# Performance work log

Measured on AMD Instinct MI355X. Metric: run time of the kernel, lower is better.

Reference implementation:

```python
import jax, jax.numpy as jnp
import numpy as np

D = 1024
H = 16
DH = D // H  # 64


def setup_inputs() -> dict:
    key = jax.random.key(0)
    ks = jax.random.split(key, 11)
    B, T = 4, 2048
    s = 1.0 / np.sqrt(D)
    return {
        "q": jax.random.normal(ks[0], (B, T, D), jnp.float32),
        "k": jax.random.normal(ks[1], (B, T, D), jnp.float32),
        "v": jax.random.normal(ks[2], (B, T, D), jnp.float32),
        "Wq": jax.random.normal(ks[3], (D, D), jnp.float32) * s,
        "bq": jnp.zeros((D,), jnp.float32),
        "Wk": jax.random.normal(ks[4], (D, D), jnp.float32) * s,
        "bk": jnp.zeros((D,), jnp.float32),
        "Wv": jax.random.normal(ks[5], (D, D), jnp.float32) * s,
        "bv": jnp.zeros((D,), jnp.float32),
        "gamma": jnp.ones((D,), jnp.float32),
        "beta": jnp.zeros((D,), jnp.float32),
    }


def _layernorm(x, gamma, beta, eps=1e-8):
    # torch LayerNorm variant: unbiased std, eps added to std (not var)
    mean = jnp.mean(x, axis=-1, keepdims=True)
    var = jnp.sum((x - mean) ** 2, axis=-1, keepdims=True) / (x.shape[-1] - 1)
    std = jnp.sqrt(var)
    return gamma * (x - mean) / (std + eps) + beta


def reference(q, k, v, Wq, bq, Wk, bk, Wv, bv, gamma, beta):
    B, T, _ = q.shape
    # projections (D -> D)
    q_ = q @ Wq + bq
    k_ = k @ Wk + bk
    v_ = v @ Wv + bv
    # head split: chunk(dim=2) + cat(dim=0)  ==  (B,T,H,dh) -> (H,B,T,dh)
    qh = q_.reshape(B, T, H, DH).transpose(2, 0, 1, 3)
    kh = k_.reshape(B, T, H, DH).transpose(2, 0, 1, 3)
    vh = v_.reshape(B, T, H, DH).transpose(2, 0, 1, 3)
    scores = jnp.einsum("hbqd,hbkd->hbqk", qh, kh) / jnp.sqrt(
        jnp.asarray(DH, qh.dtype)
    )
    attn = jax.nn.softmax(scores, axis=-1)
    out = jnp.einsum("hbqk,hbkd->hbqd", attn, vh)  # (H,B,T,dh)
    # merge heads: chunk(dim=0) + cat(dim=2)
    out = out.transpose(1, 2, 0, 3).reshape(B, T, D)
    return _layernorm(out + q, gamma, beta)
```

## Files before the change

kernel.cpp:

```cpp
#include <hip/hip_runtime.h>

constexpr int B  = 4;
constexpr int T  = 2048;
constexpr int D  = 1024;
constexpr int H  = 16;
constexpr int DH = 64;
constexpr int BT = B * T;


typedef __attribute__((ext_vector_type(8))) short bf16x8;
typedef __attribute__((ext_vector_type(4))) float f32x4;
typedef __attribute__((ext_vector_type(4))) unsigned short u16x4;
typedef __attribute__((ext_vector_type(4))) unsigned int u32x4;

static __device__ __forceinline__ unsigned short f2bf(float f) {
    unsigned u = __builtin_bit_cast(unsigned, f);
    unsigned r = (u + 0x7fffu + ((u >> 16) & 1u)) >> 16;
    return (unsigned short)r;
}

static __device__ __forceinline__ unsigned cvt_pk_bf16(float lo, float hi) {
    unsigned r;
    asm("v_cvt_pk_bf16_f32 %0, %1, %2" : "=v"(r) : "v"(lo), "v"(hi));
    return r;
}

static __device__ __forceinline__ void pl32swap(unsigned &a, unsigned &b) {
    asm volatile("v_permlane32_swap_b32 %0, %1" : "+v"(a), "+v"(b));
}
static __device__ __forceinline__ void pl16swap(unsigned &a, unsigned &b) {
    asm volatile("v_permlane16_swap_b32 %0, %1" : "+v"(a), "+v"(b));
}

static __device__ __forceinline__ void stage16(const unsigned short* g, unsigned short* l) {
    __builtin_amdgcn_global_load_lds(
        (const __attribute__((address_space(1))) unsigned int*)g,
        (__attribute__((address_space(3))) unsigned int*)l, 16, 0, 0);
}

__global__ __launch_bounds__(256) void transpose_w(
    const float* __restrict__ Wq,
    const float* __restrict__ Wk,
    const float* __restrict__ Wv,
    unsigned short* __restrict__ WT) {
    __shared__ unsigned short tile[32][33];
    const float* src = (blockIdx.y == 0) ? Wq : (blockIdx.y == 1) ? Wk : Wv;
    unsigned short* dst = WT + (size_t)blockIdx.y * D * D;
    int tx = blockIdx.x % (D / 32);
    int ty = blockIdx.x / (D / 32);
    int c  = threadIdx.x & 31;
    int r0 = threadIdx.x >> 5;
#pragma unroll
    for (int i = 0; i < 4; i++) {
        int r = r0 + i * 8;
        tile[r][c] = f2bf(src[(size_t)(ty * 32 + r) * D + tx * 32 + c]);
    }
    __syncthreads();
#pragma unroll
    for (int i = 0; i < 4; i++) {
        int r = r0 + i * 8;
        dst[(size_t)(tx * 32 + r) * D + ty * 32 + c] = tile[c][r];
    }
}

__global__ __launch_bounds__(256, 4) void qkv_gemm_fused(
    const float* __restrict__ Xq,
    const float* __restrict__ Xk,
    const float* __restrict__ Xv,
    const unsigned short* __restrict__ WTall,
    const float* __restrict__ bq,
    const float* __restrict__ bk,
    const float* __restrict__ bv,
    unsigned short* __restrict__ Qp,
    unsigned short* __restrict__ Kp,
    unsigned short* __restrict__ Vt) {
    __shared__ __align__(16) unsigned short Als[128 * 64];
    __shared__ __align__(16) unsigned short Bls[128 * 64];

    const int which = blockIdx.y;
    const float* X = (which == 0) ? Xq : (which == 1) ? Xk : Xv;
    const unsigned short* Wt = WTall + (size_t)which * D * D;
    const float* bias = (which == 0) ? bq : (which == 1) ? bk : bv;

    int bx = blockIdx.x;
    int sb   = (bx & 7) * 64 + (bx >> 3);
    int nblk = sb & 7;
    int mblk = sb >> 3;
    int tid  = threadIdx.x;
    int wave = tid >> 6, lane = tid & 63;
    int lane15 = lane & 15, quad = lane >> 4;
    int wm = (wave >> 1) * 64;
    int wn = (wave & 1) * 64;

    const size_t m0 = (size_t)mblk * 128;
    const size_t n0 = (size_t)nblk * 128;

    f32x4 acc[4][4] = {};

    for (int kt = 0; kt < D / 64; kt++) {
        int k0 = kt * 64;
#pragma unroll
        for (int i = 0; i < 4; i++) {
            int gl  = i * 256 + tid;
            int row = gl >> 3, c = gl & 7;
            int sg  = c ^ (row & 7);
            stage16(Wt + (n0 + row) * D + k0 + sg * 8,
                    Bls + (size_t)(i * 256 + wave * 64) * 8);
        }
        f32x4 xa[4][2];
#pragma unroll
        for (int j = 0; j < 4; j++) {
            int id  = j * 256 + tid;
            int row = id >> 3, c = id & 7;
            int sg  = c ^ (row & 7);
            const float* src = X + (m0 + row) * D + k0 + sg * 8;
            xa[j][0] = *(const f32x4*)(src);
            xa[j][1] = *(const f32x4*)(src + 4);
        }
#pragma unroll
        for (int j = 0; j < 4; j++) {
            int id = j * 256 + tid;
            u32x4 w;
            w[0] = cvt_pk_bf16(xa[j][0][0], xa[j][0][1]);
            w[1] = cvt_pk_bf16(xa[j][0][2], xa[j][0][3]);
            w[2] = cvt_pk_bf16(xa[j][1][0], xa[j][1][1]);
            w[3] = cvt_pk_bf16(xa[j][1][2], xa[j][1][3]);
            *(bf16x8*)(Als + (size_t)id * 8) = __builtin_bit_cast(bf16x8, w);
        }
        __syncthreads();

        bf16x8 af[2][4], bfr[2][4];
#pragma unroll
        for (int h = 0; h < 2; h++) {
#pragma unroll
            for (int i = 0; i < 4; i++) {
                int rowa = wm + i * 16 + lane15;
                int ga   = (h * 4 + quad) ^ (rowa & 7);
                af[h][i] = *(const bf16x8*)(Als + (size_t)rowa * 64 + ga * 8);
                int rowb = wn + i * 16 + lane15;
                int gb   = (h * 4 + quad) ^ (rowb & 7);
                bfr[h][i] = *(const bf16x8*)(Bls + (size_t)rowb * 64 + gb * 8);
            }
        }
#pragma unroll
        for (int h = 0; h < 2; h++)
#pragma unroll
            for (int mi = 0; mi < 4; mi++)
#pragma unroll
                for (int nf = 0; nf < 4; nf++)
                    acc[mi][nf] = __builtin_amdgcn_mfma_f32_16x16x32_bf16(
                        af[h][mi], bfr[h][nf], acc[mi][nf], 0, 0, 0);
        __syncthreads();
    }

    const float scl = (which == 0) ? 0.18033688011112042f : 1.0f;
    if (which == 2) {
#pragma unroll
        for (int nf = 0; nf < 4; nf++) {
            int n = nblk * 128 + wn + nf * 16 + lane15;
            float bn = bias[n];
            int h = n >> 6, d = n & 63;
#pragma unroll
            for (int mi = 0; mi < 4; mi++) {
                int t0 = mblk * 128 + wm + mi * 16 + quad * 4;
                int b_ = t0 >> 11;
                int tt = t0 & (T - 1);
                u16x4 o;
#pragma unroll
                for (int r = 0; r < 4; r++) o[r] = f2bf(acc[mi][nf][r] + bn);
                *(u16x4*)(Vt + (size_t)((b_ * H + h) * DH + d) * T + tt) = o;
            }
        }
    } else {
        unsigned short* P = (which == 0) ? Qp : Kp;
#pragma unroll
        for (int nf = 0; nf < 4; nf++) {
            int n = nblk * 128 + wn + nf * 16 + lane15;
            float bn = bias[n];
            int h = n >> 6, d = n & 63;
#pragma unroll
            for (int mi = 0; mi < 4; mi++) {
#pragma unroll
                for (int r = 0; r < 4; r++) {
                    int m  = mblk * 128 + wm + mi * 16 + quad * 4 + r;
                    int b_ = m >> 11;
                    int t  = m & (T - 1);
                    P[(size_t)((b_ * H + h) * T + t) * DH + d] =
                        f2bf((acc[mi][nf][r] + bn) * scl);
                }
            }
        }
    }
}

__global__ __launch_bounds__(256, 2) void attn_kernel(
    const unsigned short* __restrict__ Qp,
    const unsigned short* __restrict__ Kp,
    const unsigned short* __restrict__ Vt,
    float* __restrict__ AO) {
    __shared__ __align__(16) unsigned short Kls[2][64 * 64];
    __shared__ __align__(16) unsigned short Vls[2][64 * 64];

    constexpr int NT = T / 64;

    int bx = blockIdx.x;
    int sb = (bx & 7) * 128 + (bx >> 3);
    int qt = sb & 15;
    int bh = sb >> 4;

    int tid  = threadIdx.x;
    int wave = tid >> 6, lane = tid & 63;
    int lane15 = lane & 15, quad = lane >> 4;

    const unsigned short* Qb = Qp + (size_t)bh * T * DH;
    const unsigned short* Kb = Kp + (size_t)bh * T * DH;
    const unsigned short* Vb = Vt + (size_t)bh * DH * T;

    int qbase = qt * 128 + wave * 32;
    bf16x8 qa[2][2];
#pragma unroll
    for (int mi = 0; mi < 2; mi++)
#pragma unroll
        for (int hh = 0; hh < 2; hh++)
            qa[mi][hh] = *(const bf16x8*)(
                Qb + (size_t)(qbase + mi * 16 + lane15) * DH + hh * 32 + quad * 8);

    float ps[2] = {0.f, 0.f};
    f32x4 O[2][4] = {};

#pragma unroll
    for (int i = 0; i < 2; i++) {
        int gl = i * 256 + tid;
        int row = gl >> 3, c = gl & 7;
        int sg = c ^ (row & 7);
        stage16(Kb + (size_t)row * DH + sg * 8,
                &Kls[0][(size_t)(i * 256 + wave * 64) * 8]);
        stage16(Vb + (size_t)row * T + sg * 8,
                &Vls[0][(size_t)(i * 256 + wave * 64) * 8]);
    }
    __syncthreads();

    int cur = 0;
    for (int kt = 0; kt < NT; kt++) {
        if (kt + 1 < NT) {
            int nkb = (kt + 1) * 64;
#pragma unroll
            for (int i = 0; i < 2; i++) {
                int gl = i * 256 + tid;
                int row = gl >> 3, c = gl & 7;
                int sg = c ^ (row & 7);
                stage16(Kb + (size_t)(nkb + row) * DH + sg * 8,
                        &Kls[cur ^ 1][(size_t)(i * 256 + wave * 64) * 8]);
                stage16(Vb + (size_t)row * T + nkb + sg * 8,
                        &Vls[cur ^ 1][(size_t)(i * 256 + wave * 64) * 8]);
            }
        }

        bf16x8 kf[4][2];
#pragma unroll
        for (int nf = 0; nf < 4; nf++) {
            int r = nf * 16 + lane15;
#pragma unroll
            for (int hh = 0; hh < 2; hh++) {
                int ch = (hh * 4 + quad) ^ (r & 7);
                kf[nf][hh] = *(const bf16x8*)(&Kls[cur][(size_t)r * 64 + ch * 8]);
            }
        }

        f32x4 st[4][2] = {};
        __builtin_amdgcn_s_setprio(1);
#pragma unroll
        for (int nf = 0; nf < 4; nf++)
#pragma unroll
            for (int mi = 0; mi < 2; mi++) {
                st[nf][mi] = __builtin_amdgcn_mfma_f32_16x16x32_bf16(
                    kf[nf][0], qa[mi][0], st[nf][mi], 0, 0, 0);
                st[nf][mi] = __builtin_amdgcn_mfma_f32_16x16x32_bf16(
                    kf[nf][1], qa[mi][1], st[nf][mi], 0, 0, 0);
            }
        __builtin_amdgcn_s_setprio(0);

        unsigned e[4][2][2];
#pragma unroll
        for (int nf = 0; nf < 4; nf++)
#pragma unroll
            for (int mi = 0; mi < 2; mi++) {
                f32x4 p;
#pragma unroll
                for (int r = 0; r < 4; r++) {
                    p[r] = __builtin_amdgcn_exp2f(st[nf][mi][r]);
                    ps[mi] += p[r];
                }
                e[nf][mi][0] = cvt_pk_bf16(p[0], p[1]);
                e[nf][mi][1] = cvt_pk_bf16(p[2], p[3]);
            }

        bf16x8 vf[4][2];
#pragma unroll
        for (int nf = 0; nf < 4; nf++) {
            int r = nf * 16 + lane15;
#pragma unroll
            for (int hh = 0; hh < 2; hh++) {
                int ch = (hh * 4 + quad) ^ (r & 7);
                vf[nf][hh] = *(const bf16x8*)(&Vls[cur][(size_t)r * 64 + ch * 8]);
            }
        }

        __builtin_amdgcn_s_setprio(1);
#pragma unroll
        for (int mi = 0; mi < 2; mi++) {
#pragma unroll
            for (int ks = 0; ks < 2; ks++) {
                unsigned a0 = e[2 * ks][mi][0], b0 = e[2 * ks + 1][mi][0];
                pl32swap(a0, b0);
                pl16swap(a0, b0);
                unsigned a1 = e[2 * ks][mi][1], b1 = e[2 * ks + 1][mi][1];
                pl32swap(a1, b1);
                pl16swap(a1, b1);
                u32x4 w;
                w[0] = a0; w[1] = a1; w[2] = b0; w[3] = b1;
                bf16x8 pa = __builtin_bit_cast(bf16x8, w);
#pragma unroll
                for (int nf = 0; nf < 4; nf++)
                    O[mi][nf] = __builtin_amdgcn_mfma_f32_16x16x32_bf16(
                        pa, vf[nf][ks], O[mi][nf], 0, 0, 0);
            }
        }
        __builtin_amdgcn_s_setprio(0);

        __syncthreads();
        cur ^= 1;
    }

    float dinv[2][4];
#pragma unroll
    for (int mi = 0; mi < 2; mi++) {
        ps[mi] += __shfl_xor(ps[mi], 16);
        ps[mi] += __shfl_xor(ps[mi], 32);
        float iv = 1.0f / ps[mi];
#pragma unroll
        for (int r = 0; r < 4; r++)
            dinv[mi][r] = __shfl(iv, (lane & 48) + ((lane >> 4) & 3) * 4 + r);
    }

    int hd = bh & 15;
    int b_ = bh >> 4;
#pragma unroll
    for (int mi = 0; mi < 2; mi++) {
#pragma unroll
        for (int r = 0; r < 4; r++) {
            int t = qbase + mi * 16 + quad * 4 + r;
            float* dst = AO + (size_t)(b_ * T + t) * D + hd * DH;
#pragma unroll
            for (int nf = 0; nf < 4; nf++) {
                dst[nf * 16 + lane15] = O[mi][nf][r] * dinv[mi][r];
            }
        }
    }
}

__global__ __launch_bounds__(256) void ln_kernel(
    float* io,
    const float* __restrict__ qin,
    const float* __restrict__ gamma,
    const float* __restrict__ beta) {
    int row = blockIdx.x;
    int tid = threadIdx.x;
    size_t base = (size_t)row * D + tid * 4;
    f32x4 xo = *(const f32x4*)(io + base);
    f32x4 xq = *(const f32x4*)(qin + base);
    f32x4 x;
    float sum = 0.f, ss = 0.f;
#pragma unroll
    for (int i = 0; i < 4; i++) {
        x[i] = xo[i] + xq[i];
        sum += x[i];
        ss += x[i] * x[i];
    }
#pragma unroll
    for (int off = 32; off >= 1; off >>= 1) {
        sum += __shfl_xor(sum, off);
        ss  += __shfl_xor(ss, off);
    }
    __shared__ float s1[4], s2[4];
    int wave = tid >> 6, lane = tid & 63;
    if (lane == 0) { s1[wave] = sum; s2[wave] = ss; }
    __syncthreads();
    sum = s1[0] + s1[1] + s1[2] + s1[3];
    ss  = s2[0] + s2[1] + s2[2] + s2[3];
    float mean = sum * (1.0f / D);
    float var  = (ss - sum * mean) * (1.0f / (D - 1));
    var = fmaxf(var, 0.0f);
    float inv = 1.0f / (sqrtf(var) + 1e-8f);
    f32x4 g = *(const f32x4*)(gamma + tid * 4);
    f32x4 bb = *(const f32x4*)(beta + tid * 4);
    f32x4 o;
#pragma unroll
    for (int i = 0; i < 4; i++) o[i] = g[i] * (x[i] - mean) * inv + bb[i];
    *(f32x4*)(io + base) = o;
}

extern "C" void kernel_launch(void* const* d_in, const int* in_sizes, int n_in,
                              void* d_out, int out_size, void* d_ws, size_t ws_size,
                              hipStream_t stream) {
    (void)in_sizes; (void)n_in; (void)out_size; (void)ws_size;
    const float* xin[3] = {(const float*)d_in[0], (const float*)d_in[1], (const float*)d_in[2]};
    const float* Wq  = (const float*)d_in[3];
    const float* bq  = (const float*)d_in[4];
    const float* Wk  = (const float*)d_in[5];
    const float* bk  = (const float*)d_in[6];
    const float* Wv  = (const float*)d_in[7];
    const float* bv  = (const float*)d_in[8];
    const float* gam = (const float*)d_in[9];
    const float* bet = (const float*)d_in[10];
    float* out = (float*)d_out;

    unsigned short* ws = (unsigned short*)d_ws;
    unsigned short* Qp = ws;
    unsigned short* Kp = Qp + (size_t)BT * D;
    unsigned short* Vt = Kp + (size_t)BT * D;
    unsigned short* WT = (unsigned short*)d_out;

    transpose_w<<<dim3((D / 32) * (D / 32), 3), 256, 0, stream>>>(Wq, Wk, Wv, WT);
    qkv_gemm_fused<<<dim3((BT / 128) * (D / 128), 3), 256, 0, stream>>>(
        xin[0], xin[1], xin[2], WT, bq, bk, bv, Qp, Kp, Vt);
    attn_kernel<<<dim3(B * H * (T / 128)), 256, 0, stream>>>(Qp, Kp, Vt, out);
    ln_kernel<<<dim3(BT), 256, 0, stream>>>(out, xin[0], gam, bet);
}
```

Measured before the change: 321.1 us.

## Software-pipeline QKV GEMM with double-buffered weight tiles and register-prefetched activations

Restructures the QKV projection GEMM main loop so the next k-tile's weight tile is staged into a second LDS buffer and the next activation tile is loaded into registers while MFMAs run on the current tile. The activation tile is converted to bf16 and written to LDS after the compute, behind an extra barrier. This aims to hide global load latency behind matrix math. In exchange it uses more LDS and registers, drops launch bounds occupancy from 4 to 3 blocks per CU, and adds a second barrier per iteration.

```diff
diff --git a/kernel.cpp b/kernel.cpp
--- a/kernel.cpp
+++ b/kernel.cpp
@@ -63,7 +63,7 @@
     }
 }
 
-__global__ __launch_bounds__(256, 4) void qkv_gemm_fused(
+__global__ __launch_bounds__(256, 3) void qkv_gemm_fused(
     const float* __restrict__ Xq,
     const float* __restrict__ Xk,
     const float* __restrict__ Xv,
@@ -75,7 +75,7 @@
     unsigned short* __restrict__ Kp,
     unsigned short* __restrict__ Vt) {
     __shared__ __align__(16) unsigned short Als[128 * 64];
-    __shared__ __align__(16) unsigned short Bls[128 * 64];
+    __shared__ __align__(16) unsigned short Bls[2][128 * 64];
 
     const int which = blockIdx.y;
     const float* X = (which == 0) ? Xq : (which == 1) ? Xk : Xv;
@@ -95,39 +95,53 @@
     const size_t m0 = (size_t)mblk * 128;
     const size_t n0 = (size_t)nblk * 128;
 
+    int srow[4], ssg[4];
+#pragma unroll
+    for (int j = 0; j < 4; j++) {
+        int id  = j * 256 + tid;
+        srow[j] = id >> 3;
+        ssg[j]  = (id & 7) ^ (srow[j] & 7);
+    }
+
     f32x4 acc[4][4] = {};
-
+    f32x4 xa[4][2];
+
+#pragma unroll
+    for (int j = 0; j < 4; j++)
+        stage16(Wt + (n0 + srow[j]) * D + ssg[j] * 8,
+                Bls[0] + (size_t)(j * 256 + wave * 64) * 8);
+#pragma unroll
+    for (int j = 0; j < 4; j++) {
+        const float* src = X + (m0 + srow[j]) * D + ssg[j] * 8;
+        xa[j][0] = *(const f32x4*)(src);
+        xa[j][1] = *(const f32x4*)(src + 4);
+    }
+#pragma unroll
+    for (int j = 0; j < 4; j++) {
+        u32x4 w;
+        w[0] = cvt_pk_bf16(xa[j][0][0], xa[j][0][1]);
+        w[1] = cvt_pk_bf16(xa[j][0][2], xa[j][0][3]);
+        w[2] = cvt_pk_bf16(xa[j][1][0], xa[j][1][1]);
+        w[3] = cvt_pk_bf16(xa[j][1][2], xa[j][1][3]);
+        *(bf16x8*)(Als + (size_t)(j * 256 + tid) * 8) = __builtin_bit_cast(bf16x8, w);
+    }
+    __syncthreads();
+
+    int c = 0;
     for (int kt = 0; kt < D / 64; kt++) {
-        int k0 = kt * 64;
-#pragma unroll
-        for (int i = 0; i < 4; i++) {
-            int gl  = i * 256 + tid;
-            int row = gl >> 3, c = gl & 7;
-            int sg  = c ^ (row & 7);
-            stage16(Wt + (n0 + row) * D + k0 + sg * 8,
-                    Bls + (size_t)(i * 256 + wave * 64) * 8);
-        }
-        f32x4 xa[4][2];
-#pragma unroll
-        for (int j = 0; j < 4; j++) {
-            int id  = j * 256 + tid;
-            int row = id >> 3, c = id & 7;
-            int sg  = c ^ (row & 7);
-            const float* src = X + (m0 + row) * D + k0 + sg * 8;
-            xa[j][0] = *(const f32x4*)(src);
-            xa[j][1] = *(const f32x4*)(src + 4);
-        }
-#pragma unroll
-        for (int j = 0; j < 4; j++) {
-            int id = j * 256 + tid;
-            u32x4 w;
-            w[0] = cvt_pk_bf16(xa[j][0][0], xa[j][0][1]);
-            w[1] = cvt_pk_bf16(xa[j][0][2], xa[j][0][3]);
-            w[2] = cvt_pk_bf16(xa[j][1][0], xa[j][1][1]);
-            w[3] = cvt_pk_bf16(xa[j][1][2], xa[j][1][3]);
-            *(bf16x8*)(Als + (size_t)id * 8) = __builtin_bit_cast(bf16x8, w);
-        }
-        __syncthreads();
+        if (kt + 1 < D / 64) {
+            int kn = (kt + 1) * 64;
+#pragma unroll
+            for (int j = 0; j < 4; j++)
+                stage16(Wt + (n0 + srow[j]) * D + kn + ssg[j] * 8,
+                        Bls[c ^ 1] + (size_t)(j * 256 + wave * 64) * 8);
+#pragma unroll
+            for (int j = 0; j < 4; j++) {
+                const float* src = X + (m0 + srow[j]) * D + kn + ssg[j] * 8;
+                xa[j][0] = *(const f32x4*)(src);
+                xa[j][1] = *(const f32x4*)(src + 4);
+            }
+        }
 
         bf16x8 af[2][4], bfr[2][4];
 #pragma unroll
@@ -139,7 +153,7 @@
                 af[h][i] = *(const bf16x8*)(Als + (size_t)rowa * 64 + ga * 8);
                 int rowb = wn + i * 16 + lane15;
                 int gb   = (h * 4 + quad) ^ (rowb & 7);
-                bfr[h][i] = *(const bf16x8*)(Bls + (size_t)rowb * 64 + gb * 8);
+                bfr[h][i] = *(const bf16x8*)(Bls[c] + (size_t)rowb * 64 + gb * 8);
             }
         }
 #pragma unroll
@@ -150,7 +164,22 @@
                 for (int nf = 0; nf < 4; nf++)
                     acc[mi][nf] = __builtin_amdgcn_mfma_f32_16x16x32_bf16(
                         af[h][mi], bfr[h][nf], acc[mi][nf], 0, 0, 0);
+
         __syncthreads();
+
+        if (kt + 1 < D / 64) {
+#pragma unroll
+            for (int j = 0; j < 4; j++) {
+                u32x4 w;
+                w[0] = cvt_pk_bf16(xa[j][0][0], xa[j][0][1]);
+                w[1] = cvt_pk_bf16(xa[j][0][2], xa[j][0][3]);
+                w[2] = cvt_pk_bf16(xa[j][1][0], xa[j][1][1]);
+                w[3] = cvt_pk_bf16(xa[j][1][2], xa[j][1][3]);
+                *(bf16x8*)(Als + (size_t)(j * 256 + tid) * 8) = __builtin_bit_cast(bf16x8, w);
+            }
+            __syncthreads();
+        }
+        c ^= 1;
     }
 
     const float scl = (which == 0) ? 0.18033688011112042f : 1.0f;
```

Measured after the change: 317.9 us. Within noise of the previous version (-1.0%).
